# Kernel tuning notes

Hardware: AMD Instinct MI355X
Metric: run time of the kernel (lower is better)

Reference implementation:

```python
import jax, jax.numpy as jnp
import numpy as np

N = 100000      # entities
E = 400000      # triples (KG1)
EH = 400000     # half of symmetric all-edge list
R = 2000        # relations (rel1_size)
RH = 100        # r_hidden
EHID = 300      # e_hidden
LGE = 60000     # line-graph edges
NEG_SLOPE = 0.01


def seg_softmax(e, idx, num):
    # PyG-style segment softmax with max-subtraction and +1e-16 denom
    m = jax.ops.segment_max(e, idx, num_segments=num)
    p = jnp.exp(e - m[idx])
    s = jax.ops.segment_sum(p, idx, num_segments=num)
    return p / (s[idx] + 1e-16)


def gcn(x, w, ei):
    j, i = ei[0], ei[1]
    deg = jax.ops.segment_sum(jnp.ones(ei.shape[1], x.dtype), i, num_segments=x.shape[0])
    dinv = jnp.where(deg > 0, deg ** -0.5, 0.0)
    norm = dinv[j] * dinv[i]                       # [E]
    xw = x @ w.T                                   # [N,300]
    out = jax.ops.segment_sum(norm[:, None] * xw[j], i, num_segments=x.shape[0])
    return jax.nn.relu(out)


def highway(x1, x2, w, b):
    g = jax.nn.sigmoid(x1 @ w.T + b)
    return g * x2 + (1.0 - g) * x1


def l_gat(x, ei, val):
    j, i = ei[0], ei[1]
    n = x.shape[0]
    vi = seg_softmax(val, i, n)
    vj = seg_softmax(val, j, n)
    alpha = seg_softmax(vi + vj, j, n)
    return jax.nn.relu(jax.ops.segment_sum(alpha[:, None] * x[j], i, num_segments=n))


def gat(x, r_emb, ei, rel_e, a_i, a_j, a_r):
    j, i = ei[0], ei[1]
    e = (x @ a_i)[i] + (x @ a_j)[j] + (r_emb @ a_r)[rel_e]
    alpha = seg_softmax(jax.nn.leaky_relu(e, NEG_SLOPE), i, x.shape[0])
    return jax.nn.relu(jax.ops.segment_sum(alpha[:, None] * x[j], i, num_segments=x.shape[0]))


def gat_r_to_e(x_e, x_r, ei, rel_e, a_h, a_t, a_r):
    h, t = ei[0], ei[1]
    n_e = x_e.shape[0]
    eh = (x_e @ a_h)[h]
    et = (x_e @ a_t)[t]
    er = (x_r @ a_r)[rel_e]
    a1 = seg_softmax(jax.nn.leaky_relu(eh + er, NEG_SLOPE), h, n_e)
    x_h = jax.ops.segment_sum(a1[:, None] * x_r[rel_e], h, num_segments=n_e)
    a2 = seg_softmax(jax.nn.leaky_relu(et + er, NEG_SLOPE), t, n_e)
    x_t = jax.ops.segment_sum(a2[:, None] * x_r[rel_e], t, num_segments=n_e)
    return jnp.concatenate([x_h, x_t], axis=1)


def setup_inputs() -> dict:
    key = jax.random.key(0)
    ks = jax.random.split(key, 24)
    # symmetric all-edge graph (guarantees nonzero degrees at touched nodes)
    src = jax.random.randint(ks[0], (EH,), 0, N, dtype=jnp.int32)
    dst = jax.random.randint(ks[1], (EH,), 0, N, dtype=jnp.int32)
    edge_index_all = jnp.stack([jnp.concatenate([src, dst]), jnp.concatenate([dst, src])])
    rel_all = jax.random.randint(ks[2], (2 * EH,), 0, 2 * R, dtype=jnp.int32)
    edge_index = jnp.stack([jax.random.randint(ks[3], (E,), 0, N, dtype=jnp.int32),
                            jax.random.randint(ks[4], (E,), 0, N, dtype=jnp.int32)])
    rel = jax.random.randint(ks[5], (E,), 0, R, dtype=jnp.int32)
    lg_merge = jax.random.randint(ks[6], (2, LGE), 0, R, dtype=jnp.int32)
    lg_triangular = jax.random.randint(ks[7], (2, LGE), 0, R, dtype=jnp.int32)
    merge_val = jax.random.normal(ks[8], (LGE,), jnp.float32)
    tri_val = jax.random.normal(ks[9], (LGE,), jnp.float32)
    x_e = jax.random.normal(ks[10], (N, EHID), jnp.float32)
    s = 0.05
    return {
        'x_e': x_e, 'merge_val': merge_val, 'tri_val': tri_val,
        'gcn1_w': s * jax.random.normal(ks[11], (EHID, EHID), jnp.float32),
        'hw1_w': s * jax.random.normal(ks[12], (EHID, EHID), jnp.float32),
        'hw1_b': jnp.zeros((EHID,), jnp.float32),
        'gcn2_w': s * jax.random.normal(ks[13], (EHID, EHID), jnp.float32),
        'hw2_w': s * jax.random.normal(ks[14], (EHID, EHID), jnp.float32),
        'hw2_b': jnp.zeros((EHID,), jnp.float32),
        'rel_emb_out1': s * jax.random.normal(ks[15], (R, RH), jnp.float32),
        'rel_emb_tri1': s * jax.random.normal(ks[16], (R, RH), jnp.float32),
        'hwr_w': s * jax.random.normal(ks[17], (RH, RH), jnp.float32),
        'hwr_b': jnp.zeros((RH,), jnp.float32),
        'gat_ai': s * jax.random.normal(ks[18], (EHID,), jnp.float32),
        'gat_aj': s * jax.random.normal(ks[19], (EHID,), jnp.float32),
        'gat_ar': s * jax.random.normal(ks[20], (2 * RH,), jnp.float32),
        'g2e_ah': s * jax.random.normal(ks[21], (2 * EHID,), jnp.float32),
        'g2e_at': s * jax.random.normal(ks[22], (2 * EHID,), jnp.float32),
        'g2e_ar': s * jax.random.normal(ks[23], (RH,), jnp.float32),
        'edge_index': edge_index, 'rel': rel,
        'edge_index_all': edge_index_all, 'rel_all': rel_all,
        'lg_merge': lg_merge, 'lg_triangular': lg_triangular,
    }


def reference(x_e, merge_val, tri_val, gcn1_w, hw1_w, hw1_b, gcn2_w, hw2_w, hw2_b,
              rel_emb_out1, rel_emb_tri1, hwr_w, hwr_b, gat_ai, gat_aj, gat_ar,
              g2e_ah, g2e_at, g2e_ar, edge_index, rel, edge_index_all, rel_all,
              lg_merge, lg_triangular):
    x = highway(x_e, gcn(x_e, gcn1_w, edge_index_all), hw1_w, hw1_b)
    x = highway(x, gcn(x, gcn2_w, edge_index_all), hw2_w, hw2_b)
    # rel.max()+1 == rel1_size branch (KG1)
    rel_merge = l_gat(rel_emb_out1, lg_merge, merge_val)      # [R,RH]
    rel_tri = l_gat(rel_emb_tri1, lg_triangular, tri_val)     # [R,RH]
    x_r = highway(rel_merge, rel_tri, hwr_w, hwr_b)           # [R,RH]
    rel_cat = jnp.concatenate([rel_merge, rel_tri], axis=1)   # [R,2RH]
    rel_emb = jnp.concatenate([rel_cat, rel_cat], axis=0)     # [2R,2RH]
    x = jnp.concatenate([x, gat(x, rel_emb, edge_index_all, rel_all, gat_ai, gat_aj, gat_ar)], axis=1)  # [N,600]
    x = jnp.concatenate([x, gat_r_to_e(x, x_r, edge_index, rel, g2e_ah, g2e_at, g2e_ar)], axis=1)        # [N,800]
    return x
```

## Files before the change

kernel.cpp:

```cpp
#include <hip/hip_runtime.h>

#define WAVE 64
#define CDIV(a,b) (((a)+(b)-1)/(b))
#define XBS 320

typedef float f32x16 __attribute__((ext_vector_type(16)));
typedef unsigned short u16x8 __attribute__((ext_vector_type(8)));

__device__ __forceinline__ unsigned short f2bf_rne(float f) {
    unsigned u = __float_as_uint(f);
    unsigned r = (u + 0x7FFFu + ((u >> 16) & 1u)) >> 16;
    return (unsigned short)r;
}
__device__ __forceinline__ float bf2f(unsigned short h) {
    return __uint_as_float(((unsigned)h) << 16);
}
__device__ __forceinline__ float2 bfp2f(ushort2 u) {
    float2 r; r.x = bf2f(u.x); r.y = bf2f(u.y); return r;
}
__device__ __forceinline__ float sigm(float x) { return 1.0f / (1.0f + expf(-x)); }

#define MFMA32(acc, a, b) \
    asm volatile("v_mfma_f32_32x32x16_bf16 %0, %1, %2, %0" : "+v"(acc) : "v"(a), "v"(b))

__device__ __forceinline__ unsigned f2mono(float f) {
    unsigned u = __float_as_uint(f);
    return (u & 0x80000000u) ? ~u : (u | 0x80000000u);
}
__device__ __forceinline__ float mono2f(unsigned u) {
    return (u & 0x80000000u) ? __uint_as_float(u & 0x7fffffffu) : __uint_as_float(~u);
}
__device__ __forceinline__ float leaky(float v) { return (v > 0.0f) ? v : 0.01f*v; }

__device__ __forceinline__ long fragoff(long r, int k, int npk) {
    return ((r >> 5) * (long)npk + (k >> 4)) * 512
         + (((k >> 3) & 1) << 8) + ((r & 31) << 3) + (k & 7);
}

__global__ void k_cvt_pack1(const float* __restrict__ src, long ld, int rows, int K, int npk,
                            int roff, unsigned short* __restrict__ dst)
{
    int nc4 = npk << 2;
    long idx = (long)blockIdx.x*blockDim.x + threadIdx.x;
    if (idx >= (long)rows * nc4) return;
    long r = idx / nc4; int k = (int)(idx % nc4) << 2;
    float4 v = {0.0f, 0.0f, 0.0f, 0.0f};
    if (k + 4 <= K) v = *(const float4*)(src + r*ld + k);
    ushort4 h;
    h.x = f2bf_rne(v.x); h.y = f2bf_rne(v.y); h.z = f2bf_rne(v.z); h.w = f2bf_rne(v.w);
    *(ushort4*)(dst + fragoff(r + roff, k, npk)) = h;
}

__global__ void k_cvt_w4(const float* __restrict__ g1w, const float* __restrict__ h1w,
                         const float* __restrict__ g2w, const float* __restrict__ h2w,
                         int npk, unsigned short* __restrict__ W0,
                         unsigned short* __restrict__ W1)
{
    const int nc4 = npk << 2;
    const long per = (long)300 * nc4;
    long idx = (long)blockIdx.x*blockDim.x + threadIdx.x;
    if (idx >= 4*per) return;
    int which = (int)(idx / per);
    long lidx = idx % per;
    long r = lidx / nc4; int k = (int)(lidx % nc4) << 2;
    const float* src = (which == 0) ? g1w : (which == 1) ? h1w : (which == 2) ? g2w : h2w;
    unsigned short* dst = (which < 2) ? W0 : W1;
    int roff = (which & 1) ? 320 : 0;
    float4 v = {0.0f, 0.0f, 0.0f, 0.0f};
    if (k + 4 <= 300) v = *(const float4*)(src + r*300 + k);
    ushort4 h;
    h.x = f2bf_rne(v.x); h.y = f2bf_rne(v.y); h.z = f2bf_rne(v.z); h.w = f2bf_rne(v.w);
    *(ushort4*)(dst + fragoff(r + roff, k, npk)) = h;
}

__global__ __launch_bounds__(256, 3)
void k_gemm_frag(const unsigned short* __restrict__ Ab,
                 const unsigned short* __restrict__ Bb,
                 unsigned short* __restrict__ C, long ldc, int M, int N, int nk, int nrb)
{
    const int lane = threadIdx.x & 63;
    const int wid  = threadIdx.x >> 6;
    const int lin  = blockIdx.x;
    const int xcd  = lin & 7;
    const int m    = lin >> 3;
    const int col0 = (m % 5) * 128;
    const int rb   = xcd + ((m / 5) << 3);
    if (rb >= nrb) return;
    const int row0 = rb * 128 + wid * 32;

    const long cs = (long)nk * 512;
    const unsigned short* pA = Ab + (long)(row0 >> 5) * cs + lane * 8;
    const unsigned short* pB = Bb + (long)(col0 >> 5) * cs + lane * 8;

    f32x16 acc[4];
    #pragma unroll
    for (int c = 0; c < 4; ++c) acc[c] = (f32x16)0.0f;

    u16x8 pa, pb0, pb1, pb2, pb3;
    u16x8 qa, qb0, qb1, qb2, qb3;

    #define LOADP(t_) { long o = (long)(t_)*512;                                   \
        pa  = *(const u16x8*)(pA + o);                                             \
        pb0 = *(const u16x8*)(pB + o);        pb1 = *(const u16x8*)(pB + cs + o);  \
        pb2 = *(const u16x8*)(pB + 2*cs + o); pb3 = *(const u16x8*)(pB + 3*cs + o); }
    #define LOADQ(t_) { long o = (long)(t_)*512;                                   \
        qa  = *(const u16x8*)(pA + o);                                             \
        qb0 = *(const u16x8*)(pB + o);        qb1 = *(const u16x8*)(pB + cs + o);  \
        qb2 = *(const u16x8*)(pB + 2*cs + o); qb3 = *(const u16x8*)(pB + 3*cs + o); }
    #define STEPP {                                                                 \
        MFMA32(acc[0], pa, pb0); MFMA32(acc[1], pa, pb1);                           \
        MFMA32(acc[2], pa, pb2); MFMA32(acc[3], pa, pb3); }
    #define STEPQ {                                                                 \
        MFMA32(acc[0], qa, qb0); MFMA32(acc[1], qa, qb1);                           \
        MFMA32(acc[2], qa, qb2); MFMA32(acc[3], qa, qb3); }

    LOADP(0);
    int t = 0;
    for (;;) {
        bool m1 = (t + 1 < nk);
        if (m1) LOADQ(t + 1);
        STEPP;
        if (!m1) break;
        bool m2 = (t + 2 < nk);
        if (m2) LOADP(t + 2);
        STEPQ;
        if (!m2) break;
        t += 2;
    }
    #undef LOADP
    #undef LOADQ
    #undef STEPP
    #undef STEPQ

    const int crow0 = row0 + 4*(lane >> 5);
    const int ccol0 = col0 + (lane & 31);
    #pragma unroll
    for (int c = 0; c < 4; ++c) {
        int col = ccol0 + c*32;
        if (col >= N) continue;
        #pragma unroll
        for (int reg = 0; reg < 16; ++reg) {
            int row = crow0 + (reg & 3) + 8*(reg >> 2);
            if (row < M) C[(long)row*ldc + col] = f2bf_rne(acc[c][reg]);
        }
    }
}

#define GBM 64
#define GBN 64
#define GBK 16
__global__ __launch_bounds__(256)
void k_gemm(const float* __restrict__ A, long lda,
            const float* __restrict__ B, long ldb,
            float* __restrict__ C, long ldc,
            int M, int N, int K)
{
    __shared__ float As[GBK][GBM + 4];
    __shared__ float Bs[GBK][GBN + 4];
    const int tid = threadIdx.x;
    const int tx = tid & 15, ty = tid >> 4;
    const int row0 = blockIdx.y * GBM, col0 = blockIdx.x * GBN;
    float acc[4][4] = {};
    for (int kt = 0; kt < K; kt += GBK) {
        #pragma unroll
        for (int p = 0; p < 4; ++p) {
            int mn = (tid >> 4) + p * 16;
            int k  = tid & 15;
            int gk = kt + k;
            int gr = row0 + mn;
            As[k][mn] = (gr < M && gk < K) ? A[(long)gr * lda + gk] : 0.0f;
            int gc = col0 + mn;
            Bs[k][mn] = (gc < N && gk < K) ? B[(long)gc * ldb + gk] : 0.0f;
        }
        __syncthreads();
        #pragma unroll
        for (int kk = 0; kk < GBK; ++kk) {
            float a0 = As[kk][ty*4+0], a1 = As[kk][ty*4+1];
            float a2 = As[kk][ty*4+2], a3 = As[kk][ty*4+3];
            float b0 = Bs[kk][tx*4+0], b1 = Bs[kk][tx*4+1];
            float b2 = Bs[kk][tx*4+2], b3 = Bs[kk][tx*4+3];
            acc[0][0] += a0*b0; acc[0][1] += a0*b1; acc[0][2] += a0*b2; acc[0][3] += a0*b3;
            acc[1][0] += a1*b0; acc[1][1] += a1*b1; acc[1][2] += a1*b2; acc[1][3] += a1*b3;
            acc[2][0] += a2*b0; acc[2][1] += a2*b1; acc[2][2] += a2*b2; acc[2][3] += a2*b3;
            acc[3][0] += a3*b0; acc[3][1] += a3*b1; acc[3][2] += a3*b2; acc[3][3] += a3*b3;
        }
        __syncthreads();
    }
    #pragma unroll
    for (int i2 = 0; i2 < 4; ++i2)
        #pragma unroll
        for (int j2 = 0; j2 < 4; ++j2) {
            int r = row0 + ty*4 + i2, c = col0 + tx*4 + j2;
            if (r < M && c < N) C[(long)r*ldc + c] = acc[i2][j2];
        }
}

__global__ void k_hist3(const int* __restrict__ iA, const int* __restrict__ hE,
                        const int* __restrict__ tE, int* __restrict__ cnt,
                        int EA, int E, int N) {
    int e = blockIdx.x*blockDim.x + threadIdx.x;
    int tot = EA + 2*E;
    if (e >= tot) return;
    if (e < EA)            atomicAdd(&cnt[iA[e]], 1);
    else if (e < EA + E)   atomicAdd(&cnt[N + hE[e - EA]], 1);
    else                   atomicAdd(&cnt[2*N + tE[e - EA - E]], 1);
}
__global__ void k_scan1(const int* __restrict__ in, int* __restrict__ out,
                        int* __restrict__ bsum, int n) {
    __shared__ int sh[512];
    int gid = blockIdx.x*512 + threadIdx.x;
    int v = (gid < n) ? in[gid] : 0;
    sh[threadIdx.x] = v; __syncthreads();
    for (int o = 1; o < 512; o <<= 1) {
        int t = (threadIdx.x >= o) ? sh[threadIdx.x - o] : 0;
        __syncthreads();
        sh[threadIdx.x] += t;
        __syncthreads();
    }
    if (gid < n) out[gid] = sh[threadIdx.x] - v;
    if (threadIdx.x == 511) bsum[blockIdx.x] = sh[511];
}
__global__ void k_scan2(int* __restrict__ bsum, int nb) {
    __shared__ int sh[1024];
    int v = (threadIdx.x < nb) ? bsum[threadIdx.x] : 0;
    sh[threadIdx.x] = v; __syncthreads();
    for (int o = 1; o < 1024; o <<= 1) {
        int t = (threadIdx.x >= o) ? sh[threadIdx.x - o] : 0;
        __syncthreads();
        sh[threadIdx.x] += t;
        __syncthreads();
    }
    if (threadIdx.x < nb) bsum[threadIdx.x] = sh[threadIdx.x] - v;
}
__global__ void k_scan3(int* __restrict__ out, const int* __restrict__ bsum, int n) {
    int gid = blockIdx.x*512 + threadIdx.x;
    if (gid < n) out[gid] += bsum[blockIdx.x];
}
__global__ void k_fill3f(const int* __restrict__ iA, const int* __restrict__ jA,
                         const int* __restrict__ hE, const int* __restrict__ tE,
                         const int* __restrict__ rel_all, const int* __restrict__ rel,
                         const int* __restrict__ rowptr, const int* __restrict__ cnt,
                         int* __restrict__ cursor,
                         int* __restrict__ jp, float* __restrict__ nm,
                         int* __restrict__ relp,
                         int EA, int E, int N, int R) {
    int e = blockIdx.x*blockDim.x + threadIdx.x;
    int tot = EA + 2*E;
    if (e >= tot) return;
    if (e < EA) {
        int le = e;
        int i = iA[le];
        int p = rowptr[i] + atomicAdd(&cursor[i], 1);
        int j = jA[le];
        jp[p] = j;
        float di = rsqrtf((float)cnt[i]);
        int cj = cnt[j];
        float dj = (cj > 0) ? rsqrtf((float)cj) : 0.0f;
        nm[p] = di * dj;
        relp[p] = rel_all[le] % R;
    } else if (e < EA + E) {
        int le = e - EA;
        int key = N + hE[le];
        int p = rowptr[key] + atomicAdd(&cursor[key], 1);
        relp[p] = rel[le];
    } else {
        int le = e - EA - E;
        int key = 2*N + tE[le];
        int p = rowptr[key] + atomicAdd(&cursor[key], 1);
        relp[p] = rel[le];
    }
}

__global__ void k_gather_hw(const unsigned short* __restrict__ xg, long ldx,
                            const unsigned short* __restrict__ gl,
                            const float* __restrict__ x1f,
                            const unsigned short* __restrict__ x1b,
                            const float* __restrict__ bias,
                            const int* __restrict__ jp, const float* __restrict__ nm,
                            const int* __restrict__ rowptr, const int* __restrict__ cnt,
                            float* __restrict__ outp, long ldo,
                            unsigned short* __restrict__ pk,
                            unsigned short* __restrict__ xbf,
                            const float* __restrict__ ai, const float* __restrict__ aj,
                            float* __restrict__ sa, float* __restrict__ sb,
                            int npk, int n)
{
    int w = (blockIdx.x*blockDim.x + threadIdx.x) >> 6;
    int lane = threadIdx.x & 63;
    if (w >= n) return;
    int beg = rowptr[w], end = beg + cnt[w];
    const int i0 = lane, i1 = lane + 64, i2 = lane + 128;
    const bool t3 = (lane < 22);
    float2 a0 = {0,0}, a1 = {0,0}, a2 = {0,0};
    int e = beg;
    for (; e + 8 <= end; e += 8) {
        long jj[8]; float wt[8];
        #pragma unroll
        for (int u = 0; u < 8; ++u) { jj[u] = jp[e+u]; wt[u] = nm[e+u]; }
        #pragma unroll
        for (int u = 0; u < 8; ++u) {
            float2 v = bfp2f(((const ushort2*)(xg + jj[u]*ldx))[i0]);
            a0.x += wt[u]*v.x; a0.y += wt[u]*v.y;
        }
        #pragma unroll
        for (int u = 0; u < 8; ++u) {
            float2 v = bfp2f(((const ushort2*)(xg + jj[u]*ldx))[i1]);
            a1.x += wt[u]*v.x; a1.y += wt[u]*v.y;
        }
        if (t3) {
            #pragma unroll
            for (int u = 0; u < 8; ++u) {
                float2 v = bfp2f(((const ushort2*)(xg + jj[u]*ldx))[i2]);
                a2.x += wt[u]*v.x; a2.y += wt[u]*v.y;
            }
        }
    }
    for (; e + 4 <= end; e += 4) {
        long jj[4]; float wt[4];
        #pragma unroll
        for (int u = 0; u < 4; ++u) { jj[u] = jp[e+u]; wt[u] = nm[e+u]; }
        #pragma unroll
        for (int u = 0; u < 4; ++u) {
            float2 v = bfp2f(((const ushort2*)(xg + jj[u]*ldx))[i0]);
            a0.x += wt[u]*v.x; a0.y += wt[u]*v.y;
        }
        #pragma unroll
        for (int u = 0; u < 4; ++u) {
            float2 v = bfp2f(((const ushort2*)(xg + jj[u]*ldx))[i1]);
            a1.x += wt[u]*v.x; a1.y += wt[u]*v.y;
        }
        if (t3) {
            #pragma unroll
            for (int u = 0; u < 4; ++u) {
                float2 v = bfp2f(((const ushort2*)(xg + jj[u]*ldx))[i2]);
                a2.x += wt[u]*v.x; a2.y += wt[u]*v.y;
            }
        }
    }
    for (; e < end; ++e) {
        long j0 = jp[e]; float w0 = nm[e];
        float2 v;
        v = bfp2f(((const ushort2*)(xg + j0*ldx))[i0]); a0.x += w0*v.x; a0.y += w0*v.y;
        v = bfp2f(((const ushort2*)(xg + j0*ldx))[i1]); a1.x += w0*v.x; a1.y += w0*v.y;
        if (t3) { v = bfp2f(((const ushort2*)(xg + j0*ldx))[i2]); a2.x += w0*v.x; a2.y += w0*v.y; }
    }
    const ushort2* glr = (const ushort2*)(gl + (long)w*ldx);
    const float2*  x1r = (const float2*)(x1f + (long)w*300);
    const ushort2* x1r2 = (const ushort2*)(x1b + (long)w*XBS);
    const float2*  br  = (const float2*)bias;
    float2 o0 = {0,0}, o1 = {0,0}, o2 = {0,0};
    {
        float2 gv = bfp2f(glr[i0]); float2 bv = br[i0];
        float2 xv = x1f ? x1r[i0] : bfp2f(x1r2[i0]);
        float g0 = sigm(gv.x + bv.x), g1 = sigm(gv.y + bv.y);
        o0.x = g0*fmaxf(a0.x,0.0f) + (1.0f-g0)*xv.x;
        o0.y = g1*fmaxf(a0.y,0.0f) + (1.0f-g1)*xv.y;
    }
    {
        float2 gv = bfp2f(glr[i1]); float2 bv = br[i1];
        float2 xv = x1f ? x1r[i1] : bfp2f(x1r2[i1]);
        float g0 = sigm(gv.x + bv.x), g1 = sigm(gv.y + bv.y);
        o1.x = g0*fmaxf(a1.x,0.0f) + (1.0f-g0)*xv.x;
        o1.y = g1*fmaxf(a1.y,0.0f) + (1.0f-g1)*xv.y;
    }
    if (t3) {
        float2 gv = bfp2f(glr[i2]); float2 bv = br[i2];
        float2 xv = x1f ? x1r[i2] : bfp2f(x1r2[i2]);
        float g0 = sigm(gv.x + bv.x), g1 = sigm(gv.y + bv.y);
        o2.x = g0*fmaxf(a2.x,0.0f) + (1.0f-g0)*xv.x;
        o2.y = g1*fmaxf(a2.y,0.0f) + (1.0f-g1)*xv.y;
    }
    if (outp) {
        float2* dst = (float2*)(outp + (long)w*ldo);
        dst[i0] = o0; dst[i1] = o1;
        if (t3) dst[i2] = o2;
    }
    if (pk) {
        auto pack2 = [&](int k, float2 o) {
            ushort2 hv; hv.x = f2bf_rne(o.x); hv.y = f2bf_rne(o.y);
            *(ushort2*)(pk + fragoff(w, k, npk)) = hv;
        };
        pack2(2*lane, o0);
        pack2(128 + 2*lane, o1);
        if (t3) pack2(256 + 2*lane, o2);
        else if (lane < 24) {
            ushort2 z = {0,0};
            *(ushort2*)(pk + fragoff(w, 256 + 2*lane, npk)) = z;
        }
    }
    if (xbf) {
        ushort2* xw = (ushort2*)(xbf + (long)w*XBS);
        ushort2 t;
        t.x = f2bf_rne(o0.x); t.y = f2bf_rne(o0.y); xw[i0] = t;
        t.x = f2bf_rne(o1.x); t.y = f2bf_rne(o1.y); xw[i1] = t;
        if (t3) { t.x = f2bf_rne(o2.x); t.y = f2bf_rne(o2.y); xw[i2] = t; }
    }
    if (sa) {
        const float2* ai2 = (const float2*)ai;
        const float2* aj2 = (const float2*)aj;
        float2 A0 = ai2[i0], A1 = ai2[i1], J0 = aj2[i0], J1 = aj2[i1];
        float sva = o0.x*A0.x + o0.y*A0.y + o1.x*A1.x + o1.y*A1.y;
        float svb = o0.x*J0.x + o0.y*J0.y + o1.x*J1.x + o1.y*J1.y;
        if (t3) {
            float2 A2 = ai2[i2], J2 = aj2[i2];
            sva += o2.x*A2.x + o2.y*A2.y;
            svb += o2.x*J2.x + o2.y*J2.y;
        }
        #pragma unroll
        for (int o = 32; o > 0; o >>= 1) {
            sva += __shfl_down(sva, o);
            svb += __shfl_down(svb, o);
        }
        if (lane == 0) { sa[w] = sva; sb[w] = svb; }
    }
}

__global__ void k_gat300(const unsigned short* __restrict__ xbf,
                         const float* __restrict__ sA, const float* __restrict__ sB,
                         const float* __restrict__ rsc,
                         const int* __restrict__ jp, const int* __restrict__ relp,
                         const int* __restrict__ rowptr, const int* __restrict__ cnt,
                         float* __restrict__ out, long ldo,
                         const float* __restrict__ ah, const float* __restrict__ at,
                         float* __restrict__ sh, float* __restrict__ st,
                         int n)
{
    int w = (blockIdx.x*blockDim.x + threadIdx.x) >> 6;
    int lane = threadIdx.x & 63;
    if (w >= n) return;
    int beg = rowptr[w], c = cnt[w];
    const int i0 = lane, i1 = lane + 64, i2 = lane + 128;
    const bool t3 = (lane < 22);
    float2 a0 = {0,0}, a1 = {0,0}, a2 = {0,0};
    if (c > 0) {
        float base = sA[w];
        int   jc = 0;
        float sval = -3.4e38f;
        if (lane < c) {
            jc = jp[beg + lane];
            sval = leaky(base + sB[jc] + rsc[relp[beg + lane]]);
        }
        float mx = sval;
        for (int t = 64 + lane; t < c; t += 64)
            mx = fmaxf(mx, leaky(base + sB[jp[beg+t]] + rsc[relp[beg+t]]));
        #pragma unroll
        for (int o = 32; o > 0; o >>= 1) mx = fmaxf(mx, __shfl_xor(mx, o));
        float pexp = (lane < c) ? expf(sval - mx) : 0.0f;
        float ss = pexp;
        for (int t = 64 + lane; t < c; t += 64)
            ss += expf(leaky(base + sB[jp[beg+t]] + rsc[relp[beg+t]]) - mx);
        #pragma unroll
        for (int o = 32; o > 0; o >>= 1) ss += __shfl_xor(ss, o);
        float inv = 1.0f / (ss + 1e-16f);
        int q = 0;
        int cc = (c < 64) ? c : 64;
        for (; q + 8 <= cc; q += 8) {
            float al[8]; long jj[8];
            #pragma unroll
            for (int u = 0; u < 8; ++u) {
                al[u] = __shfl(pexp, q+u) * inv;
                jj[u] = __shfl(jc, q+u);
            }
            #pragma unroll
            for (int u = 0; u < 8; ++u) {
                float2 v = bfp2f(((const ushort2*)(xbf + jj[u]*XBS))[i0]);
                a0.x += al[u]*v.x; a0.y += al[u]*v.y;
            }
            #pragma unroll
            for (int u = 0; u < 8; ++u) {
                float2 v = bfp2f(((const ushort2*)(xbf + jj[u]*XBS))[i1]);
                a1.x += al[u]*v.x; a1.y += al[u]*v.y;
            }
            if (t3) {
                #pragma unroll
                for (int u = 0; u < 8; ++u) {
                    float2 v = bfp2f(((const ushort2*)(xbf + jj[u]*XBS))[i2]);
                    a2.x += al[u]*v.x; a2.y += al[u]*v.y;
                }
            }
        }
        for (; q + 4 <= cc; q += 4) {
            float al[4]; long jj[4];
            #pragma unroll
            for (int u = 0; u < 4; ++u) {
                al[u] = __shfl(pexp, q+u) * inv;
                jj[u] = __shfl(jc, q+u);
            }
            #pragma unroll
            for (int u = 0; u < 4; ++u) {
                float2 v = bfp2f(((const ushort2*)(xbf + jj[u]*XBS))[i0]);
                a0.x += al[u]*v.x; a0.y += al[u]*v.y;
            }
            #pragma unroll
            for (int u = 0; u < 4; ++u) {
                float2 v = bfp2f(((const ushort2*)(xbf + jj[u]*XBS))[i1]);
                a1.x += al[u]*v.x; a1.y += al[u]*v.y;
            }
            if (t3) {
                #pragma unroll
                for (int u = 0; u < 4; ++u) {
                    float2 v = bfp2f(((const ushort2*)(xbf + jj[u]*XBS))[i2]);
                    a2.x += al[u]*v.x; a2.y += al[u]*v.y;
                }
            }
        }
        for (; q < c; ++q) {
            float al; long j0;
            if (q < 64) { al = __shfl(pexp, q) * inv; j0 = __shfl(jc, q); }
            else {
                j0 = jp[beg + q];
                al = expf(leaky(base + sB[(int)j0] + rsc[relp[beg+q]]) - mx) * inv;
            }
            float2 v;
            v = bfp2f(((const ushort2*)(xbf + j0*XBS))[i0]); a0.x += al*v.x; a0.y += al*v.y;
            v = bfp2f(((const ushort2*)(xbf + j0*XBS))[i1]); a1.x += al*v.x; a1.y += al*v.y;
            if (t3) { v = bfp2f(((const ushort2*)(xbf + j0*XBS))[i2]); a2.x += al*v.x; a2.y += al*v.y; }
        }
    }
    a0.x = fmaxf(a0.x, 0.0f); a0.y = fmaxf(a0.y, 0.0f);
    a1.x = fmaxf(a1.x, 0.0f); a1.y = fmaxf(a1.y, 0.0f);
    a2.x = fmaxf(a2.x, 0.0f); a2.y = fmaxf(a2.y, 0.0f);
    float2* dst = (float2*)(out + (long)w*ldo);
    dst[i0] = a0; dst[i1] = a1;
    if (t3) dst[i2] = a2;
    {
        const ushort2* xw = (const ushort2*)(xbf + (long)w*XBS);
        const float2* ahL = (const float2*)ah;
        const float2* atL = (const float2*)at;
        const float2* ahH = (const float2*)(ah + 300);
        const float2* atH = (const float2*)(at + 300);
        float2 x0 = bfp2f(xw[i0]), x1v = bfp2f(xw[i1]);
        float svh = x0.x*ahL[i0].x + x0.y*ahL[i0].y + x1v.x*ahL[i1].x + x1v.y*ahL[i1].y
                  + a0.x*ahH[i0].x + a0.y*ahH[i0].y + a1.x*ahH[i1].x + a1.y*ahH[i1].y;
        float svt = x0.x*atL[i0].x + x0.y*atL[i0].y + x1v.x*atL[i1].x + x1v.y*atL[i1].y
                  + a0.x*atH[i0].x + a0.y*atH[i0].y + a1.x*atH[i1].x + a1.y*atH[i1].y;
        if (t3) {
            float2 x2v = bfp2f(xw[i2]);
            svh += x2v.x*ahL[i2].x + x2v.y*ahL[i2].y + a2.x*ahH[i2].x + a2.y*ahH[i2].y;
            svt += x2v.x*atL[i2].x + x2v.y*atL[i2].y + a2.x*atH[i2].x + a2.y*atH[i2].y;
        }
        #pragma unroll
        for (int o = 32; o > 0; o >>= 1) {
            svh += __shfl_down(svh, o);
            svt += __shfl_down(svt, o);
        }
        if (lane == 0) { sh[w] = svh; st[w] = svt; }
    }
}

__global__ void k_gather_rel2(const unsigned short* __restrict__ xrb,
                              const float* __restrict__ sH, const float* __restrict__ sT,
                              const float* __restrict__ srel,
                              const int* __restrict__ relp,
                              const int* __restrict__ rowptrH, const int* __restrict__ cntH,
                              const int* __restrict__ rowptrT, const int* __restrict__ cntT,
                              float* __restrict__ out, long ldo, int n)
{
    int gw = (blockIdx.x*blockDim.x + threadIdx.x) >> 6;
    int lane = threadIdx.x & 63;
    if (gw >= 2*n) return;
    const bool isT = (gw >= n);
    const int w = isT ? gw - n : gw;
    const float* snode = isT ? sT : sH;
    const int* rowptr = isT ? rowptrT : rowptrH;
    const int* cnt    = isT ? cntT    : cntH;
    float* dst = out + (isT ? 700 : 600) + (long)w*ldo;
    int beg = rowptr[w], c = cnt[w];
    const bool t0 = (lane < 50);
    float2 a0 = {0,0};
    if (c > 0) {
        float base = snode[w];
        int   rc = 0;
        float sval = -3.4e38f;
        if (lane < c) {
            rc = relp[beg + lane];
            sval = leaky(base + srel[rc]);
        }
        float mx = sval;
        for (int t = 64 + lane; t < c; t += 64)
            mx = fmaxf(mx, leaky(base + srel[relp[beg+t]]));
        #pragma unroll
        for (int o = 32; o > 0; o >>= 1) mx = fmaxf(mx, __shfl_xor(mx, o));
        float pexp = (lane < c) ? expf(sval - mx) : 0.0f;
        float ss = pexp;
        for (int t = 64 + lane; t < c; t += 64)
            ss += expf(leaky(base + srel[relp[beg+t]]) - mx);
        #pragma unroll
        for (int o = 32; o > 0; o >>= 1) ss += __shfl_xor(ss, o);
        float inv = 1.0f / (ss + 1e-16f);
        int q = 0;
        int cc = (c < 64) ? c : 64;
        for (; q + 4 <= cc; q += 4) {
            float al0 = __shfl(pexp, q)   * inv;
            float al1 = __shfl(pexp, q+1) * inv;
            float al2 = __shfl(pexp, q+2) * inv;
            float al3 = __shfl(pexp, q+3) * inv;
            long r0i = __shfl(rc, q), r1i = __shfl(rc, q+1);
            long r2i = __shfl(rc, q+2), r3i = __shfl(rc, q+3);
            if (t0) {
                float2 v;
                v = bfp2f(((const ushort2*)(xrb + r0i*128))[lane]); a0.x += al0*v.x; a0.y += al0*v.y;
                v = bfp2f(((const ushort2*)(xrb + r1i*128))[lane]); a0.x += al1*v.x; a0.y += al1*v.y;
                v = bfp2f(((const ushort2*)(xrb + r2i*128))[lane]); a0.x += al2*v.x; a0.y += al2*v.y;
                v = bfp2f(((const ushort2*)(xrb + r3i*128))[lane]); a0.x += al3*v.x; a0.y += al3*v.y;
            }
        }
        for (; q < c; ++q) {
            float al; long r0i;
            if (q < 64) { al = __shfl(pexp, q) * inv; r0i = __shfl(rc, q); }
            else {
                r0i = relp[beg + q];
                al = expf(leaky(base + srel[(int)r0i]) - mx) * inv;
            }
            if (t0) {
                float2 v = bfp2f(((const ushort2*)(xrb + r0i*128))[lane]);
                a0.x += al*v.x; a0.y += al*v.y;
            }
        }
    }
    if (t0) ((float2*)dst)[lane] = a0;
}

__global__ void k_lgat_max(const float* __restrict__ mval, const float* __restrict__ tval,
                           const int* __restrict__ iM, const int* __restrict__ jM,
                           const int* __restrict__ iT, const int* __restrict__ jT,
                           unsigned* __restrict__ mi, unsigned* __restrict__ mj,
                           int LGE, int R)
{
    int e = blockIdx.x*blockDim.x + threadIdx.x;
    if (e >= 2*LGE) return;
    bool g1 = e >= LGE; int le = g1 ? e - LGE : e;
    float v = g1 ? tval[le] : mval[le];
    int i = (g1 ? iT[le] : iM[le]) + (g1 ? R : 0);
    int j = (g1 ? jT[le] : jM[le]) + (g1 ? R : 0);
    unsigned mv = f2mono(v);
    atomicMax(&mi[i], mv);
    atomicMax(&mj[j], mv);
}
__global__ void k_lgat_sum(const float* __restrict__ mval, const float* __restrict__ tval,
                           const int* __restrict__ iM, const int* __restrict__ jM,
                           const int* __restrict__ iT, const int* __restrict__ jT,
                           const unsigned* __restrict__ mi, const unsigned* __restrict__ mj,
                           float* __restrict__ si, float* __restrict__ sj,
                           int LGE, int R)
{
    int e = blockIdx.x*blockDim.x + threadIdx.x;
    if (e >= 2*LGE) return;
    bool g1 = e >= LGE; int le = g1 ? e - LGE : e;
    float v = g1 ? tval[le] : mval[le];
    int i = (g1 ? iT[le] : iM[le]) + (g1 ? R : 0);
    int j = (g1 ? jT[le] : jM[le]) + (g1 ? R : 0);
    atomicAdd(&si[i], expf(v - mono2f(mi[i])));
    atomicAdd(&sj[j], expf(v - mono2f(mj[j])));
}
__global__ void k_lgat_vsum2(const float* __restrict__ mval, const float* __restrict__ tval,
                             const int* __restrict__ iM, const int* __restrict__ jM,
                             const int* __restrict__ iT, const int* __restrict__ jT,
                             const unsigned* __restrict__ mi, const float* __restrict__ si,
                             const unsigned* __restrict__ mj, const float* __restrict__ sj,
                             float* __restrict__ vsum, int LGE, int R)
{
    int e = blockIdx.x*blockDim.x + threadIdx.x;
    if (e >= 2*LGE) return;
    bool g1 = e >= LGE; int le = g1 ? e - LGE : e;
    float v = g1 ? tval[le] : mval[le];
    int i = (g1 ? iT[le] : iM[le]) + (g1 ? R : 0);
    int j = (g1 ? jT[le] : jM[le]) + (g1 ? R : 0);
    float pi = expf(v - mono2f(mi[i])) / (si[i] + 1e-16f);
    float pj = expf(v - mono2f(mj[j])) / (sj[j] + 1e-16f);
    vsum[e] = pi + pj;
}
__global__ void k_lgat_max2(const float* __restrict__ vsum,
                            const int* __restrict__ jM, const int* __restrict__ jT,
                            unsigned* __restrict__ m2, int LGE, int R)
{
    int e = blockIdx.x*blockDim.x + threadIdx.x;
    if (e >= 2*LGE) return;
    bool g1 = e >= LGE; int le = g1 ? e - LGE : e;
    int j = (g1 ? jT[le] : jM[le]) + (g1 ? R : 0);
    atomicMax(&m2[j], f2mono(vsum[e]));
}
__global__ void k_lgat_sum2(const float* __restrict__ vsum,
                            const int* __restrict__ jM, const int* __restrict__ jT,
                            const unsigned* __restrict__ m2, float* __restrict__ s2,
                            int LGE, int R)
{
    int e = blockIdx.x*blockDim.x + threadIdx.x;
    if (e >= 2*LGE) return;
    bool g1 = e >= LGE; int le = g1 ? e - LGE : e;
    int j = (g1 ? jT[le] : jM[le]) + (g1 ? R : 0);
    atomicAdd(&s2[j], expf(vsum[e] - mono2f(m2[j])));
}
__global__ void k_lgat_agg(const float* __restrict__ vsum,
                           const unsigned* __restrict__ m2, const float* __restrict__ s2,
                           const int* __restrict__ iM, const int* __restrict__ jM,
                           const int* __restrict__ iT, const int* __restrict__ jT,
                           const float* __restrict__ remb1, const float* __restrict__ remb2,
                           float* __restrict__ obuf, int LGE, int R, int RH)
{
    int w = (blockIdx.x*blockDim.x + threadIdx.x) >> 6;
    int lane = threadIdx.x & 63;
    if (w >= 2*LGE) return;
    bool g1 = w >= LGE; int le = g1 ? w - LGE : w;
    int o = g1 ? R : 0;
    int i = (g1 ? iT[le] : iM[le]) + o;
    int j = (g1 ? jT[le] : jM[le]);
    float alpha = expf(vsum[w] - mono2f(m2[o + j])) / (s2[o + j] + 1e-16f);
    const float* x = g1 ? remb2 : remb1;
    const float4* src = (const float4*)(x + (long)j*RH);
    float* dst = obuf + (long)i*RH;
    if (lane < 25) {
        float4 v = src[lane];
        atomicAdd(&dst[lane*4+0], alpha*v.x);
        atomicAdd(&dst[lane*4+1], alpha*v.y);
        atomicAdd(&dst[lane*4+2], alpha*v.z);
        atomicAdd(&dst[lane*4+3], alpha*v.w);
    }
}
__global__ void k_relu2d(float* __restrict__ p, long rows, int cols, long ld) {
    long idx = (long)blockIdx.x*blockDim.x + threadIdx.x;
    if (idx >= rows*(long)cols) return;
    long r = idx / cols; int c = (int)(idx % cols);
    float v = p[r*ld+c];
    p[r*ld+c] = fmaxf(v, 0.0f);
}

__global__ void k_highway(const float* __restrict__ x1, long ld1,
                          const float* __restrict__ gl, long ldg,
                          const float* __restrict__ x2, long ld2,
                          const float* __restrict__ bias,
                          float* __restrict__ out, long ldo,
                          long rows, int F, int relu_x2)
{
    long idx = (long)blockIdx.x*blockDim.x + threadIdx.x;
    if (idx >= rows * (long)F) return;
    long r = idx / F; int c = (int)(idx % F);
    float g = 1.0f / (1.0f + expf(-(gl[r*ldg+c] + bias[c])));
    float v2 = x2[r*ld2+c]; if (relu_x2) v2 = fmaxf(v2, 0.0f);
    float v1 = x1[r*ld1+c];
    out[r*ldo+c] = g*v2 + (1.0f-g)*v1;
}

__global__ void k_rs2(const float* __restrict__ mg, const float* __restrict__ tr,
                      const float* __restrict__ ar,
                      const float* __restrict__ xr, const float* __restrict__ g2e_ar,
                      float* __restrict__ rsc, float* __restrict__ srel,
                      unsigned short* __restrict__ xrb, int R, int RH)
{
    int gw = (blockIdx.x*blockDim.x + threadIdx.x) >> 6;
    int lane = threadIdx.x & 63;
    if (gw >= 2*R) return;
    float s = 0.0f;
    if (gw < R) {
        for (int k = lane; k < RH; k += WAVE)
            s += mg[(long)gw*RH+k]*ar[k] + tr[(long)gw*RH+k]*ar[RH+k];
        #pragma unroll
        for (int off = 32; off > 0; off >>= 1) s += __shfl_down(s, off);
        if (lane == 0) rsc[gw] = s;
    } else {
        int r = gw - R;
        #pragma unroll
        for (int t = 0; t < 2; ++t) {
            int k = lane + t*64;
            if (k < RH) {
                float v = xr[(long)r*RH + k];
                s += v * g2e_ar[k];
                xrb[(long)r*128 + k] = f2bf_rne(v);
            }
        }
        #pragma unroll
        for (int off = 32; off > 0; off >>= 1) s += __shfl_down(s, off);
        if (lane == 0) srel[r] = s;
    }
}

extern "C" void kernel_launch(void* const* d_in, const int* in_sizes, int n_in,
                              void* d_out, int out_size, void* d_ws, size_t ws_size,
                              hipStream_t stream)
{
    const float* x_e   = (const float*)d_in[0];
    const float* mval  = (const float*)d_in[1];
    const float* tval  = (const float*)d_in[2];
    const float* g1w   = (const float*)d_in[3];
    const float* h1w   = (const float*)d_in[4];
    const float* h1b   = (const float*)d_in[5];
    const float* g2w   = (const float*)d_in[6];
    const float* h2w   = (const float*)d_in[7];
    const float* h2b   = (const float*)d_in[8];
    const float* remb1 = (const float*)d_in[9];
    const float* remb2 = (const float*)d_in[10];
    const float* hrw   = (const float*)d_in[11];
    const float* hrb   = (const float*)d_in[12];
    const float* gat_ai= (const float*)d_in[13];
    const float* gat_aj= (const float*)d_in[14];
    const float* gat_ar= (const float*)d_in[15];
    const float* g2e_ah= (const float*)d_in[16];
    const float* g2e_at= (const float*)d_in[17];
    const float* g2e_ar= (const float*)d_in[18];
    const int* edge_index     = (const int*)d_in[19];
    const int* rel            = (const int*)d_in[20];
    const int* edge_index_all = (const int*)d_in[21];
    const int* rel_all        = (const int*)d_in[22];
    const int* lg_merge       = (const int*)d_in[23];
    const int* lg_tri         = (const int*)d_in[24];

    const int F    = 300;
    const int RH   = 100;
    const int Kp   = 304;
    const int npk  = Kp / 16;
    const int N    = in_sizes[0] / F;
    const int E    = in_sizes[20];
    const int EA   = in_sizes[22];
    const int LGE  = in_sizes[1];
    const int R    = in_sizes[9] / RH;
    const long OUTC = 800;
    const int Mpad = CDIV(N, 128) * 128;
    const int NB   = 640;
    const long LDC = 640;

    const int* jA = edge_index_all;
    const int* iA = edge_index_all + EA;
    const int* hE = edge_index;
    const int* tE = edge_index + E;
    const int* jM = lg_merge;  const int* iM = lg_merge + LGE;
    const int* jT = lg_tri;    const int* iT = lg_tri  + LGE;

    float* ws = (float*)d_ws;
    size_t off = 0;
    auto alloc = [&](size_t n) { float* p = ws + off; off += (n + 15) & ~(size_t)15; return p; };
    unsigned short* Ascr = (unsigned short*)alloc((size_t)N*NB/2);
    unsigned short* Axb = (unsigned short*)alloc((size_t)Mpad*Kp/2);
    unsigned short* xbf = (unsigned short*)alloc((size_t)N*XBS/2);
    unsigned short* Wb  = (unsigned short*)alloc((size_t)2*NB*Kp/2);
    unsigned short* W0 = Wb;
    unsigned short* W1 = Wb + (size_t)NB*Kp;
    unsigned short* xrb = (unsigned short*)alloc((size_t)R*128/2);
    float*    sA_  = alloc(N);
    float*    sB_  = alloc(N);
    float*    sH_  = alloc(N);
    float*    sT_  = alloc(N);
    float*    xr   = alloc((size_t)R*RH);
    float*    xrg  = alloc((size_t)R*RH);
    float*    lg   = alloc((size_t)12*R + (size_t)2*R*RH);
    unsigned* lmi  = (unsigned*)lg;          float* lsi = lg + 2*R;
    unsigned* lmj  = (unsigned*)(lg + 4*R);  float* lsj = lg + 6*R;
    unsigned* lm2  = (unsigned*)(lg + 8*R);  float* ls2 = lg + 10*R;
    float*    obuf = lg + 12*R;
    float*    mrg  = obuf;
    float*    tri  = obuf + (size_t)R*RH;
    float*    vsum = alloc((size_t)2*LGE);
    float*    rsc  = alloc(R);
    float*    srel = alloc(R);
    int*   bsum    = (int*)alloc(1024);
    int*   cntAll  = (int*)alloc((size_t)6*N);
    int*   curAll  = cntAll + 3*N;
    int*   rowptrG = (int*)alloc((size_t)3*N);
    int*   relpAll = (int*)alloc((size_t)EA + 2*E);
    int*   jpA     = (int*)alloc(EA);
    float* nmA     = alloc(EA);

    float* out = (float*)d_out;

    const int  nrb = CDIV(N, 128);
    const int  gemmBlocks = 8 * CDIV(nrb, 8) * 5;
    const int  gatherGrid = CDIV(N, 4);
    const int  cvtBigGrid = CDIV((long)N * (Kp/4), 256);
    const int  cvtW4Grid  = CDIV((long)4 * 300 * (Kp/4), 256);
    const int  ETOT = EA + 2*E;
    const int  nb3 = CDIV(3*N, 512);

    hipMemsetAsync(Wb, 0, (size_t)2*NB*Kp*2, stream);
    hipMemsetAsync(Axb + (size_t)N*Kp, 0, (size_t)(Mpad-N)*Kp*2, stream);
    k_cvt_w4<<<cvtW4Grid,256,0,stream>>>(g1w, h1w, g2w, h2w, npk, W0, W1);
    k_cvt_pack1<<<cvtBigGrid,256,0,stream>>>(x_e, 300, N, 300, npk, 0, Axb);

    hipMemsetAsync(cntAll, 0, (size_t)6*N*4, stream);
    k_hist3<<<CDIV(ETOT,256),256,0,stream>>>(iA, hE, tE, cntAll, EA, E, N);
    k_scan1<<<nb3,512,0,stream>>>(cntAll, rowptrG, bsum, 3*N);
    k_scan2<<<1,1024,0,stream>>>(bsum, nb3);
    k_scan3<<<nb3,512,0,stream>>>(rowptrG, bsum, 3*N);
    k_fill3f<<<CDIV(ETOT,256),256,0,stream>>>(iA, jA, hE, tE, rel_all, rel,
                                              rowptrG, cntAll, curAll,
                                              jpA, nmA, relpAll, EA, E, N, R);

    k_gemm_frag<<<gemmBlocks,256,0,stream>>>(Axb, W0, Ascr, LDC, N, 620, npk, nrb);
    k_gather_hw<<<gatherGrid,256,0,stream>>>(Ascr, LDC, Ascr+320,
                                             x_e, (const unsigned short*)nullptr, h1b,
                                             jpA, nmA, rowptrG, cntAll,
                                             (float*)nullptr, OUTC, Axb, xbf,
                                             (const float*)nullptr, (const float*)nullptr,
                                             (float*)nullptr, (float*)nullptr, npk, N);

    k_gemm_frag<<<gemmBlocks,256,0,stream>>>(Axb, W1, Ascr, LDC, N, 620, npk, nrb);
    k_gather_hw<<<gatherGrid,256,0,stream>>>(Ascr, LDC, Ascr+320,
                                             (const float*)nullptr, xbf, h2b,
                                             jpA, nmA, rowptrG, cntAll,
                                             out, OUTC, (unsigned short*)nullptr, xbf,
                                             gat_ai, gat_aj, sA_, sB_, npk, N);

    hipMemsetAsync(lg, 0, ((size_t)12*R + (size_t)2*R*RH)*4, stream);
    const int lgGrid = CDIV(2*LGE, 256);
    k_lgat_max  <<<lgGrid,256,0,stream>>>(mval, tval, iM, jM, iT, jT, lmi, lmj, LGE, R);
    k_lgat_sum  <<<lgGrid,256,0,stream>>>(mval, tval, iM, jM, iT, jT, lmi, lmj, lsi, lsj, LGE, R);
    k_lgat_vsum2<<<lgGrid,256,0,stream>>>(mval, tval, iM, jM, iT, jT, lmi, lsi, lmj, lsj,
                                          vsum, LGE, R);
    k_lgat_max2 <<<lgGrid,256,0,stream>>>(vsum, jM, jT, lm2, LGE, R);
    k_lgat_sum2 <<<lgGrid,256,0,stream>>>(vsum, jM, jT, lm2, ls2, LGE, R);
    k_lgat_agg  <<<CDIV(2*LGE*64,256),256,0,stream>>>(vsum, lm2, ls2, iM, jM, iT, jT,
                                                      remb1, remb2, obuf, LGE, R, RH);
    k_relu2d    <<<CDIV((long)2*R*RH,256),256,0,stream>>>(obuf, 2*R, RH, RH);

    dim3 gridR(CDIV(RH,GBN), CDIV(R,GBM));
    k_gemm<<<gridR,256,0,stream>>>(mrg, RH, hrw, RH, xrg, RH, R, RH, RH);
    k_highway<<<CDIV((long)R*RH,256),256,0,stream>>>(mrg, RH, xrg, RH, tri, RH, hrb, xr, RH, R, RH, 0);

    k_rs2<<<CDIV((long)2*R*64,256),256,0,stream>>>(mrg, tri, gat_ar, xr, g2e_ar,
                                                   rsc, srel, xrb, R, RH);

    k_gat300<<<gatherGrid,256,0,stream>>>(xbf, sA_, sB_, rsc, jpA, relpAll,
                                          rowptrG, cntAll, out+300, OUTC,
                                          g2e_ah, g2e_at, sH_, sT_, N);

    k_gather_rel2<<<CDIV(2*N,4),256,0,stream>>>(xrb, sH_, sT_, srel, relpAll,
                                                rowptrG + N, cntAll + N,
                                                rowptrG + 2*N, cntAll + 2*N,
                                                out, OUTC, N);
}
```

Before: 1.206 ms.

## Replace atomic scatter in line-graph GAT aggregation with CSR gather

Extends the shared histogram/scan/fill CSR build to cover line-graph edges grouped by destination relation, and stores the per-edge attention logits in CSR order. The final aggregation is now one wavefront per relation that accumulates over its incoming edges in registers and applies ReLU on store. This removes the per-element float atomics into the output buffer, the separate ReLU kernel, and the zeroing of the output buffer. In exchange the CSR build kernels process more entries, an extra scattered slot index write is added, and the gather becomes serial per relation, which could be slow for high-degree relations.

After: 1.063 ms. -11.9%, faster.

```diff
diff --git a/kernel.cpp b/kernel.cpp
--- a/kernel.cpp
+++ b/kernel.cpp
@@ -195,15 +195,18 @@
         }
 }
 
-__global__ void k_hist3(const int* __restrict__ iA, const int* __restrict__ hE,
-                        const int* __restrict__ tE, int* __restrict__ cnt,
-                        int EA, int E, int N) {
+__global__ void k_hist5(const int* __restrict__ iA, const int* __restrict__ hE,
+                        const int* __restrict__ tE, const int* __restrict__ iM,
+                        const int* __restrict__ iT, int* __restrict__ cnt,
+                        int EA, int E, int LGE, int N, int R) {
     int e = blockIdx.x*blockDim.x + threadIdx.x;
-    int tot = EA + 2*E;
+    int tot = EA + 2*E + 2*LGE;
     if (e >= tot) return;
-    if (e < EA)            atomicAdd(&cnt[iA[e]], 1);
-    else if (e < EA + E)   atomicAdd(&cnt[N + hE[e - EA]], 1);
-    else                   atomicAdd(&cnt[2*N + tE[e - EA - E]], 1);
+    if (e < EA)                  atomicAdd(&cnt[iA[e]], 1);
+    else if (e < EA + E)         atomicAdd(&cnt[N + hE[e - EA]], 1);
+    else if (e < EA + 2*E)       atomicAdd(&cnt[2*N + tE[e - EA - E]], 1);
+    else if (e < EA + 2*E + LGE) atomicAdd(&cnt[3*N + iM[e - EA - 2*E]], 1);
+    else                         atomicAdd(&cnt[3*N + R + iT[e - EA - 2*E - LGE]], 1);
 }
 __global__ void k_scan1(const int* __restrict__ in, int* __restrict__ out,
                         int* __restrict__ bsum, int n) {
@@ -236,16 +239,19 @@
     int gid = blockIdx.x*512 + threadIdx.x;
     if (gid < n) out[gid] += bsum[blockIdx.x];
 }
-__global__ void k_fill3f(const int* __restrict__ iA, const int* __restrict__ jA,
+__global__ void k_fill5f(const int* __restrict__ iA, const int* __restrict__ jA,
                          const int* __restrict__ hE, const int* __restrict__ tE,
+                         const int* __restrict__ iM, const int* __restrict__ jM,
+                         const int* __restrict__ iT, const int* __restrict__ jT,
                          const int* __restrict__ rel_all, const int* __restrict__ rel,
                          const int* __restrict__ rowptr, const int* __restrict__ cnt,
                          int* __restrict__ cursor,
                          int* __restrict__ jp, float* __restrict__ nm,
                          int* __restrict__ relp,
-                         int EA, int E, int N, int R) {
+                         int* __restrict__ lgjp, int* __restrict__ slotOf,
+                         int EA, int E, int LGE, int N, int R, int lgbase) {
     int e = blockIdx.x*blockDim.x + threadIdx.x;
-    int tot = EA + 2*E;
+    int tot = EA + 2*E + 2*LGE;
     if (e >= tot) return;
     if (e < EA) {
         int le = e;
@@ -263,11 +269,23 @@
         int key = N + hE[le];
         int p = rowptr[key] + atomicAdd(&cursor[key], 1);
         relp[p] = rel[le];
-    } else {
+    } else if (e < EA + 2*E) {
         int le = e - EA - E;
         int key = 2*N + tE[le];
         int p = rowptr[key] + atomicAdd(&cursor[key], 1);
         relp[p] = rel[le];
+    } else if (e < EA + 2*E + LGE) {
+        int le = e - EA - 2*E;
+        int key = 3*N + iM[le];
+        int p = rowptr[key] + atomicAdd(&cursor[key], 1) - lgbase;
+        lgjp[p] = jM[le];
+        slotOf[le] = p;
+    } else {
+        int le = e - EA - 2*E - LGE;
+        int key = 3*N + R + iT[le];
+        int p = rowptr[key] + atomicAdd(&cursor[key], 1) - lgbase;
+        lgjp[p] = jT[le] + R;
+        slotOf[LGE + le] = p;
     }
 }
 
@@ -658,7 +676,8 @@
                              const int* __restrict__ iT, const int* __restrict__ jT,
                              const unsigned* __restrict__ mi, const float* __restrict__ si,
                              const unsigned* __restrict__ mj, const float* __restrict__ sj,
-                             float* __restrict__ vsum, int LGE, int R)
+                             const int* __restrict__ slotOf,
+                             float* __restrict__ vsumC, int LGE, int R)
 {
     int e = blockIdx.x*blockDim.x + threadIdx.x;
     if (e >= 2*LGE) return;
@@ -668,61 +687,50 @@
     int j = (g1 ? jT[le] : jM[le]) + (g1 ? R : 0);
     float pi = expf(v - mono2f(mi[i])) / (si[i] + 1e-16f);
     float pj = expf(v - mono2f(mj[j])) / (sj[j] + 1e-16f);
-    vsum[e] = pi + pj;
-}
-__global__ void k_lgat_max2(const float* __restrict__ vsum,
-                            const int* __restrict__ jM, const int* __restrict__ jT,
-                            unsigned* __restrict__ m2, int LGE, int R)
-{
-    int e = blockIdx.x*blockDim.x + threadIdx.x;
-    if (e >= 2*LGE) return;
-    bool g1 = e >= LGE; int le = g1 ? e - LGE : e;
-    int j = (g1 ? jT[le] : jM[le]) + (g1 ? R : 0);
-    atomicMax(&m2[j], f2mono(vsum[e]));
-}
-__global__ void k_lgat_sum2(const float* __restrict__ vsum,
-                            const int* __restrict__ jM, const int* __restrict__ jT,
-                            const unsigned* __restrict__ m2, float* __restrict__ s2,
-                            int LGE, int R)
-{
-    int e = blockIdx.x*blockDim.x + threadIdx.x;
-    if (e >= 2*LGE) return;
-    bool g1 = e >= LGE; int le = g1 ? e - LGE : e;
-    int j = (g1 ? jT[le] : jM[le]) + (g1 ? R : 0);
-    atomicAdd(&s2[j], expf(vsum[e] - mono2f(m2[j])));
-}
-__global__ void k_lgat_agg(const float* __restrict__ vsum,
-                           const unsigned* __restrict__ m2, const float* __restrict__ s2,
-                           const int* __restrict__ iM, const int* __restrict__ jM,
-                           const int* __restrict__ iT, const int* __restrict__ jT,
-                           const float* __restrict__ remb1, const float* __restrict__ remb2,
-                           float* __restrict__ obuf, int LGE, int R, int RH)
-{
-    int w = (blockIdx.x*blockDim.x + threadIdx.x) >> 6;
+    vsumC[slotOf[e]] = pi + pj;
+}
+__global__ void k_lgat_max2C(const float* __restrict__ vsumC, const int* __restrict__ lgjp,
+                             unsigned* __restrict__ m2, int tot)
+{
+    int p = blockIdx.x*blockDim.x + threadIdx.x;
+    if (p >= tot) return;
+    atomicMax(&m2[lgjp[p]], f2mono(vsumC[p]));
+}
+__global__ void k_lgat_sum2C(const float* __restrict__ vsumC, const int* __restrict__ lgjp,
+                             const unsigned* __restrict__ m2, float* __restrict__ s2, int tot)
+{
+    int p = blockIdx.x*blockDim.x + threadIdx.x;
+    if (p >= tot) return;
+    int j = lgjp[p];
+    atomicAdd(&s2[j], expf(vsumC[p] - mono2f(m2[j])));
+}
+__global__ void k_lgat_gather(const float* __restrict__ vsumC, const int* __restrict__ lgjp,
+                              const unsigned* __restrict__ m2, const float* __restrict__ s2,
+                              const int* __restrict__ rowptr, const int* __restrict__ cnt,
+                              const float* __restrict__ remb1, const float* __restrict__ remb2,
+                              float* __restrict__ obuf, int lgbase, int R, int RH)
+{
+    int gw = (blockIdx.x*blockDim.x + threadIdx.x) >> 6;
     int lane = threadIdx.x & 63;
-    if (w >= 2*LGE) return;
-    bool g1 = w >= LGE; int le = g1 ? w - LGE : w;
-    int o = g1 ? R : 0;
-    int i = (g1 ? iT[le] : iM[le]) + o;
-    int j = (g1 ? jT[le] : jM[le]);
-    float alpha = expf(vsum[w] - mono2f(m2[o + j])) / (s2[o + j] + 1e-16f);
-    const float* x = g1 ? remb2 : remb1;
-    const float4* src = (const float4*)(x + (long)j*RH);
-    float* dst = obuf + (long)i*RH;
-    if (lane < 25) {
-        float4 v = src[lane];
-        atomicAdd(&dst[lane*4+0], alpha*v.x);
-        atomicAdd(&dst[lane*4+1], alpha*v.y);
-        atomicAdd(&dst[lane*4+2], alpha*v.z);
-        atomicAdd(&dst[lane*4+3], alpha*v.w);
-    }
-}
-__global__ void k_relu2d(float* __restrict__ p, long rows, int cols, long ld) {
-    long idx = (long)blockIdx.x*blockDim.x + threadIdx.x;
-    if (idx >= rows*(long)cols) return;
-    long r = idx / cols; int c = (int)(idx % cols);
-    float v = p[r*ld+c];
-    p[r*ld+c] = fmaxf(v, 0.0f);
+    if (gw >= 2*R) return;
+    int beg = rowptr[gw] - lgbase, end = beg + cnt[gw];
+    float4 acc = {0,0,0,0};
+    const bool act = (lane < 25);
+    for (int p = beg; p < end; ++p) {
+        int j = lgjp[p];
+        float alpha = expf(vsumC[p] - mono2f(m2[j])) / (s2[j] + 1e-16f);
+        if (act) {
+            const float* x = (j < R) ? (remb1 + (long)j*RH) : (remb2 + (long)(j - R)*RH);
+            float4 v = ((const float4*)x)[lane];
+            acc.x += alpha*v.x; acc.y += alpha*v.y;
+            acc.z += alpha*v.z; acc.w += alpha*v.w;
+        }
+    }
+    if (act) {
+        acc.x = fmaxf(acc.x, 0.0f); acc.y = fmaxf(acc.y, 0.0f);
+        acc.z = fmaxf(acc.z, 0.0f); acc.w = fmaxf(acc.w, 0.0f);
+        ((float4*)(obuf + (long)gw*RH))[lane] = acc;
+    }
 }
 
 __global__ void k_highway(const float* __restrict__ x1, long ld1,
@@ -848,16 +856,19 @@
     float*    obuf = lg + 12*R;
     float*    mrg  = obuf;
     float*    tri  = obuf + (size_t)R*RH;
-    float*    vsum = alloc((size_t)2*LGE);
+    float*    vsumC = alloc((size_t)2*LGE);
     float*    rsc  = alloc(R);
     float*    srel = alloc(R);
     int*   bsum    = (int*)alloc(1024);
-    int*   cntAll  = (int*)alloc((size_t)6*N);
-    int*   curAll  = cntAll + 3*N;
-    int*   rowptrG = (int*)alloc((size_t)3*N);
+    const int NR   = 3*N + 2*R;
+    int*   cntAll  = (int*)alloc((size_t)2*NR);
+    int*   curAll  = cntAll + NR;
+    int*   rowptrG = (int*)alloc((size_t)NR);
     int*   relpAll = (int*)alloc((size_t)EA + 2*E);
     int*   jpA     = (int*)alloc(EA);
     float* nmA     = alloc(EA);
+    int*   lgjp    = (int*)alloc((size_t)2*LGE);
+    int*   slotOf  = (int*)alloc((size_t)2*LGE);
 
     float* out = (float*)d_out;
 
@@ -866,22 +877,24 @@
     const int  gatherGrid = CDIV(N, 4);
     const int  cvtBigGrid = CDIV((long)N * (Kp/4), 256);
     const int  cvtW4Grid  = CDIV((long)4 * 300 * (Kp/4), 256);
-    const int  ETOT = EA + 2*E;
-    const int  nb3 = CDIV(3*N, 512);
+    const int  ETOT = EA + 2*E + 2*LGE;
+    const int  lgbase = EA + 2*E;
+    const int  nbNR = CDIV(NR, 512);
 
     hipMemsetAsync(Wb, 0, (size_t)2*NB*Kp*2, stream);
     hipMemsetAsync(Axb + (size_t)N*Kp, 0, (size_t)(Mpad-N)*Kp*2, stream);
     k_cvt_w4<<<cvtW4Grid,256,0,stream>>>(g1w, h1w, g2w, h2w, npk, W0, W1);
     k_cvt_pack1<<<cvtBigGrid,256,0,stream>>>(x_e, 300, N, 300, npk, 0, Axb);
 
-    hipMemsetAsync(cntAll, 0, (size_t)6*N*4, stream);
-    k_hist3<<<CDIV(ETOT,256),256,0,stream>>>(iA, hE, tE, cntAll, EA, E, N);
-    k_scan1<<<nb3,512,0,stream>>>(cntAll, rowptrG, bsum, 3*N);
-    k_scan2<<<1,1024,0,stream>>>(bsum, nb3);
-    k_scan3<<<nb3,512,0,stream>>>(rowptrG, bsum, 3*N);
-    k_fill3f<<<CDIV(ETOT,256),256,0,stream>>>(iA, jA, hE, tE, rel_all, rel,
+    hipMemsetAsync(cntAll, 0, (size_t)2*NR*4, stream);
+    k_hist5<<<CDIV(ETOT,256),256,0,stream>>>(iA, hE, tE, iM, iT, cntAll, EA, E, LGE, N, R);
+    k_scan1<<<nbNR,512,0,stream>>>(cntAll, rowptrG, bsum, NR);
+    k_scan2<<<1,1024,0,stream>>>(bsum, nbNR);
+    k_scan3<<<nbNR,512,0,stream>>>(rowptrG, bsum, NR);
+    k_fill5f<<<CDIV(ETOT,256),256,0,stream>>>(iA, jA, hE, tE, iM, jM, iT, jT, rel_all, rel,
                                               rowptrG, cntAll, curAll,
-                                              jpA, nmA, relpAll, EA, E, N, R);
+                                              jpA, nmA, relpAll, lgjp, slotOf,
+                                              EA, E, LGE, N, R, lgbase);
 
     k_gemm_frag<<<gemmBlocks,256,0,stream>>>(Axb, W0, Ascr, LDC, N, 620, npk, nrb);
     k_gather_hw<<<gatherGrid,256,0,stream>>>(Ascr, LDC, Ascr+320,
@@ -898,17 +911,17 @@
                                              out, OUTC, (unsigned short*)nullptr, xbf,
                                              gat_ai, gat_aj, sA_, sB_, npk, N);
 
-    hipMemsetAsync(lg, 0, ((size_t)12*R + (size_t)2*R*RH)*4, stream);
+    hipMemsetAsync(lg, 0, (size_t)12*R*4, stream);
     const int lgGrid = CDIV(2*LGE, 256);
     k_lgat_max  <<<lgGrid,256,0,stream>>>(mval, tval, iM, jM, iT, jT, lmi, lmj, LGE, R);
     k_lgat_sum  <<<lgGrid,256,0,stream>>>(mval, tval, iM, jM, iT, jT, lmi, lmj, lsi, lsj, LGE, R);
     k_lgat_vsum2<<<lgGrid,256,0,stream>>>(mval, tval, iM, jM, iT, jT, lmi, lsi, lmj, lsj,
-                                          vsum, LGE, R);
-    k_lgat_max2 <<<lgGrid,256,0,stream>>>(vsum, jM, jT, lm2, LGE, R);
-    k_lgat_sum2 <<<lgGrid,256,0,stream>>>(vsum, jM, jT, lm2, ls2, LGE, R);
-    k_lgat_agg  <<<CDIV(2*LGE*64,256),256,0,stream>>>(vsum, lm2, ls2, iM, jM, iT, jT,
-                                                      remb1, remb2, obuf, LGE, R, RH);
-    k_relu2d    <<<CDIV((long)2*R*RH,256),256,0,stream>>>(obuf, 2*R, RH, RH);
+                                          slotOf, vsumC, LGE, R);
+    k_lgat_max2C<<<lgGrid,256,0,stream>>>(vsumC, lgjp, lm2, 2*LGE);
+    k_lgat_sum2C<<<lgGrid,256,0,stream>>>(vsumC, lgjp, lm2, ls2, 2*LGE);
+    k_lgat_gather<<<CDIV(2*R*64,256),256,0,stream>>>(vsumC, lgjp, lm2, ls2,
+                                                     rowptrG + 3*N, cntAll + 3*N,
+                                                     remb1, remb2, obuf, lgbase, R, RH);
 
     dim3 gridR(CDIV(RH,GBN), CDIV(R,GBM));
     k_gemm<<<gridR,256,0,stream>>>(mrg, RH, hrw, RH, xrg, RH, R, RH, RH);
```
